# Kernel tuning notes

Hardware: AMD Instinct MI355X
Metric: run time of the kernel (lower is better)

## Reference

```python
import jax, jax.numpy as jnp
import numpy as np

B, N, E = 2, 50000, 400000
C_IN, D, C, S, H, L, FFN = 5, 2, 128, 32, 8, 4, 512
COORD_F, TIME_F, FREQ_BASE, BETA = 8, 4, 1000.0, 1.0
HD = C // H


def setup_inputs() -> dict:
    key = jax.random.key(0)
    ks = jax.random.split(key, 32)
    sc = 0.02
    inp = {
        'inputs': jax.random.normal(ks[0], (B, N, C_IN), jnp.float32),
        'coords': jax.random.uniform(ks[1], (B, N, D), jnp.float32),
        't_norm': jax.random.uniform(ks[2], (B,), jnp.float32),
        'adj_indices': jax.random.randint(ks[3], (2, E), 0, N, jnp.int64 if jax.config.jax_enable_x64 else jnp.int32),
        'adj_values': jax.random.uniform(ks[4], (E,), jnp.float32) * 0.25,  # ~1/avg_degree for stable magnitudes
        'freq_matrix': jax.random.normal(ks[5], (D, COORD_F), jnp.float32),
        'embed_W': jax.random.normal(ks[6], (C_IN + 2 * COORD_F + 2 * TIME_F, C), jnp.float32) * sc,
        'embed_b': jnp.zeros((C,), jnp.float32),
        'ln1_g': jnp.ones((L, C), jnp.float32),
        'ln1_b': jnp.zeros((L, C), jnp.float32),
        'Wslice': jax.random.normal(ks[7], (L, C, S), jnp.float32) * sc,
        'bslice': jnp.zeros((L, S), jnp.float32),
        'Wfront': jax.random.normal(ks[8], (L, C, S), jnp.float32) * sc,
        'bfront': jnp.zeros((L, S), jnp.float32),
        'Win': jax.random.normal(ks[9], (L, C, 3 * C), jnp.float32) * sc,
        'b_in': jnp.zeros((L, 3 * C), jnp.float32),
        'Wout': jax.random.normal(ks[10], (L, C, C), jnp.float32) * sc,
        'bout': jnp.zeros((L, C), jnp.float32),
        'ln2_g': jnp.ones((L, C), jnp.float32),
        'ln2_b': jnp.zeros((L, C), jnp.float32),
        'Wff1': jax.random.normal(ks[11], (L, C, FFN), jnp.float32) * sc,
        'bff1': jnp.zeros((L, FFN), jnp.float32),
        'Wff2': jax.random.normal(ks[12], (L, FFN, C), jnp.float32) * sc,
        'bff2': jnp.zeros((L, C), jnp.float32),
        'proj_W': jax.random.normal(ks[13], (C, C_IN), jnp.float32) * sc,
        'proj_b': jnp.zeros((C_IN,), jnp.float32),
    }
    return inp


def _layer_norm(x, g, b, eps=1e-5):
    m = jnp.mean(x, -1, keepdims=True)
    v = jnp.mean(jnp.square(x - m), -1, keepdims=True)
    return (x - m) * jax.lax.rsqrt(v + eps) * g + b


def _forward(inputs, coords, t_norm, adj_indices, adj_values, freq_matrix,
             embed_W, embed_b, ln1_g, ln1_b, Wslice, bslice, Wfront, bfront,
             Win, b_in, Wout, bout, ln2_g, ln2_b, Wff1, bff1, Wff2, bff2,
             proj_W, proj_b):
    rows, cols = adj_indices[0], adj_indices[1]
    b, n = coords.shape[0], coords.shape[1]
    # spatial Fourier encoding (B,N,2*COORD_F)
    p = 2.0 * jnp.pi * (coords @ freq_matrix)
    sp_enc = jnp.concatenate([jnp.sin(p), jnp.cos(p)], -1)
    # temporal encoding (B,N,2*TIME_F)
    omega = FREQ_BASE ** (-jnp.arange(TIME_F, dtype=jnp.float32) / TIME_F)
    ang = omega[None, :] * (t_norm * FREQ_BASE)[:, None]
    t_enc = jnp.broadcast_to(jnp.concatenate([jnp.sin(ang), jnp.cos(ang)], -1)[:, None, :], (b, n, 2 * TIME_F))
    x = jnp.concatenate([inputs, sp_enc, t_enc], -1) @ embed_W + embed_b  # (B,N,C)
    weights_all = []
    for l in range(L):
        h = _layer_norm(x, ln1_g[l], ln1_b[l])
        # sparse adjacency aggregation: y[r] += a_e * h[c] (duplicates sum == coalesce)
        contrib = adj_values[None, :, None] * h[:, cols, :]  # (B,E,C)
        h_local = jax.vmap(lambda cb: jax.ops.segment_sum(cb, rows, num_segments=n))(contrib)
        h_front = h - h_local
        logits = h @ Wslice[l] + bslice[l] + BETA * (h_front @ Wfront[l] + bfront[l])
        w = jax.nn.softmax(logits, -1)  # (B,N,S)
        wsum = jnp.maximum(jnp.sum(w, axis=1)[:, :, None], 1e-8)  # (B,S,1)
        slices = jnp.einsum('bns,bnc->bsc', w, h) / wsum  # (B,S,C)
        # slice-space MHA (self-attention on S tokens)
        qkv = slices @ Win[l] + b_in[l]
        q, k, v = jnp.split(qkv, 3, axis=-1)
        def split_heads(t):
            return t.reshape(b, S, H, HD).transpose(0, 2, 1, 3)  # (B,H,S,HD)
        qh, kh, vh = split_heads(q), split_heads(k), split_heads(v)
        attn = jax.nn.softmax(jnp.einsum('bhqd,bhkd->bhqk', qh, kh) / jnp.sqrt(jnp.float32(HD)), -1)
        o = jnp.einsum('bhqk,bhkd->bhqd', attn, vh).transpose(0, 2, 1, 3).reshape(b, S, C)
        slices_out = o @ Wout[l] + bout[l]
        x = x + jnp.einsum('bns,bsc->bnc', w, slices_out)
        h2 = _layer_norm(x, ln2_g[l], ln2_b[l])
        x = x + jax.nn.gelu(h2 @ Wff1[l] + bff1[l], approximate=False) @ Wff2[l] + bff2[l]
        weights_all.append(w)
    out = x @ proj_W + proj_b  # (B,N,C_OUT)
    return out, jnp.stack(weights_all)  # (L,B,N,S)


def reference(inputs, coords, t_norm, adj_indices, adj_values, freq_matrix,
              embed_W, embed_b, ln1_g, ln1_b, Wslice, bslice, Wfront, bfront,
              Win, b_in, Wout, bout, ln2_g, ln2_b, Wff1, bff1, Wff2, bff2,
              proj_W, proj_b):
    return _forward(inputs, coords, t_norm, adj_indices, adj_values, freq_matrix,
                    embed_W, embed_b, ln1_g, ln1_b, Wslice, bslice, Wfront, bfront,
                    Win, b_in, Wout, bout, ln2_g, ln2_b, Wff1, bff1, Wff2, bff2,
                    proj_W, proj_b)
```

## Files before the change

### kernel.cpp

```cpp
#include <hip/hip_runtime.h>
#include <math.h>

#define BATCH 2
#define NN 50000
#define NE 400000
#define C_IN 5
#define CC 128
#define SS 32
#define NH 8
#define NL 4
#define FFN 512
#define COORD_F 8
#define TIME_F 4
#define HD 16
#define BETA 1.0f
#define TWO_PI 6.283185307179586476925287f

#define NTOT (BATCH * NN)
#define FF_MT 128
#define FF_BLOCKS ((NTOT + FF_MT - 1) / FF_MT)
#define MPAD (FF_BLOCKS * FF_MT)
#define NBLK ((NN + 127) / 128)
#define LP_PAD 136
#define H2S 136
#define HIDS 72

typedef unsigned short u16;
typedef unsigned int u32;
typedef __attribute__((ext_vector_type(8))) __bf16 bf16x8;
typedef __attribute__((ext_vector_type(4))) float f32x4;

__device__ __forceinline__ u16 f2bf(float f) {
    union { __bf16 b; u16 u; } v;
    v.b = (__bf16)f;
    return v.u;
}

__device__ __forceinline__ float bf2f(u16 h) {
    union { u32 u; float f; } v; v.u = ((u32)h) << 16;
    return v.f;
}

__device__ __forceinline__ float bf_lo(u32 u) {
    union { u32 u; float f; } v; v.u = u << 16;
    return v.f;
}

__device__ __forceinline__ float bf_hi(u32 u) {
    union { u32 u; float f; } v; v.u = u & 0xffff0000u;
    return v.f;
}

__device__ __forceinline__ float gelu_f(float a) {
    float xx = a * 0.7071067811865475f;
    float ax = fabsf(xx);
    float t = 1.0f / fmaf(0.3275911f, ax, 1.0f);
    float poly = t * fmaf(t, fmaf(t, fmaf(t, fmaf(t, 1.061405429f, -1.453152027f),
                                          1.421413741f), -0.284496736f), 0.254829592f);
    float e = __expf(-ax * ax);
    float erfv = copysignf(fmaf(-poly, e, 1.0f), xx);
    return 0.5f * a * (1.0f + erfv);
}

__global__ void count_deg(const int* rows, int* deg) {
    int e = blockIdx.x * blockDim.x + threadIdx.x;
    if (e < NE) atomicAdd(&deg[rows[e]], 1);
}

__global__ __launch_bounds__(512) void scan_deg(const int* deg, int* rowptr) {
    __shared__ int part[512];
    int t = threadIdx.x;
    const int CH = (NN + 511) / 512;
    int begin = t * CH, end = min(begin + CH, NN);
    int s = 0;
    for (int i = begin; i < end; i++) s += deg[i];
    part[t] = s;
    __syncthreads();
    for (int off = 1; off < 512; off <<= 1) {
        int v = (t >= off) ? part[t - off] : 0;
        __syncthreads();
        part[t] += v;
        __syncthreads();
    }
    int base = (t == 0) ? 0 : part[t - 1];
    for (int i = begin; i < end; i++) { rowptr[i] = base; base += deg[i]; }
    if (t == 511) rowptr[NN] = part[511];
}

__global__ void fill_csr(const int* rows, const int* cols, const float* vals,
                         int* cursor, int* csr_col, float* csr_val) {
    int e = blockIdx.x * blockDim.x + threadIdx.x;
    if (e < NE) {
        int p = atomicAdd(&cursor[rows[e]], 1);
        csr_col[p] = cols[e];
        csr_val[p] = vals[e];
    }
}

__global__ __launch_bounds__(128) void embed_ln1_kernel(const float* inputs, const float* coords,
                                                        const float* t_norm, const float* freq,
                                                        const float* W, const float* bias,
                                                        const float* g, const float* bb,
                                                        float* x, u16* hbf) {
    int node = blockIdx.x;
    int b = node / NN;
    int t = threadIdx.x;
    __shared__ float feat[32];
    __shared__ float sm[4];
    if (t < 8) {
        float c0 = coords[node * 2 + 0], c1 = coords[node * 2 + 1];
        float p = TWO_PI * (c0 * freq[t] + c1 * freq[8 + t]);
        feat[5 + t] = sinf(p);
        feat[13 + t] = cosf(p);
    } else if (t < 12) {
        int j = t - 8;
        float omega = powf(1000.0f, -(float)j * 0.25f);
        float ang = omega * t_norm[b] * 1000.0f;
        feat[21 + j] = sinf(ang);
        feat[25 + j] = cosf(ang);
    } else if (t >= 16 && t < 21) {
        feat[t - 16] = inputs[node * 5 + (t - 16)];
    }
    __syncthreads();
    float acc = bias[t];
    #pragma unroll
    for (int k = 0; k < 29; k++) acc += feat[k] * W[k * CC + t];
    x[(size_t)node * CC + t] = acc;
    float s = acc;
    #pragma unroll
    for (int off = 32; off > 0; off >>= 1) s += __shfl_xor(s, off, 64);
    if ((t & 63) == 0) sm[t >> 6] = s;
    __syncthreads();
    float mean = (sm[0] + sm[1]) * (1.0f / 128.0f);
    float d = acc - mean;
    float ss = d * d;
    #pragma unroll
    for (int off = 32; off > 0; off >>= 1) ss += __shfl_xor(ss, off, 64);
    if ((t & 63) == 0) sm[2 + (t >> 6)] = ss;
    __syncthreads();
    float var = (sm[2] + sm[3]) * (1.0f / 128.0f);
    hbf[(size_t)node * CC + t] = f2bf(d * rsqrtf(var + 1e-5f) * g[t] + bb[t]);
}

__global__ __launch_bounds__(256) void agg_kernel(const u16* __restrict__ hbf,
                                                  const int* __restrict__ rowptr,
                                                  const int* __restrict__ csr_col,
                                                  const float* __restrict__ csr_val,
                                                  u16* __restrict__ hlbf) {
    int wid = threadIdx.x >> 6;
    int lane = threadIdx.x & 63;
    int node = blockIdx.x * 4 + wid;
    int b = node / NN, r = node - b * NN;
    int s0 = rowptr[r], s1 = rowptr[r + 1];
    const u32* hb = (const u32*)(hbf + (size_t)b * NN * CC);
    float a0l = 0.f, a1l = 0.f, a2l = 0.f, a3l = 0.f;
    float a0h = 0.f, a1h = 0.f, a2h = 0.f, a3h = 0.f;
    int e = s0;
    for (; e + 4 <= s1; e += 4) {
        int c0 = csr_col[e], c1 = csr_col[e + 1], c2 = csr_col[e + 2], c3 = csr_col[e + 3];
        float v0 = csr_val[e], v1 = csr_val[e + 1], v2 = csr_val[e + 2], v3 = csr_val[e + 3];
        u32 u0 = hb[(size_t)c0 * 64 + lane];
        u32 u1 = hb[(size_t)c1 * 64 + lane];
        u32 u2 = hb[(size_t)c2 * 64 + lane];
        u32 u3 = hb[(size_t)c3 * 64 + lane];
        a0l += v0 * bf_lo(u0);  a0h += v0 * bf_hi(u0);
        a1l += v1 * bf_lo(u1);  a1h += v1 * bf_hi(u1);
        a2l += v2 * bf_lo(u2);  a2h += v2 * bf_hi(u2);
        a3l += v3 * bf_lo(u3);  a3h += v3 * bf_hi(u3);
    }
    for (; e < s1; e++) {
        float v = csr_val[e];
        u32 u = hb[(size_t)csr_col[e] * 64 + lane];
        a0l += v * bf_lo(u);  a0h += v * bf_hi(u);
    }
    float al = (a0l + a1l) + (a2l + a3l);
    float ah = (a0h + a1h) + (a2h + a3h);
    u32 outv = (u32)f2bf(al) | ((u32)f2bf(ah) << 16);
    ((u32*)hlbf)[(size_t)node * 64 + lane] = outv;
}

__global__ __launch_bounds__(256) void pack_logits_weights(const float* Ws, const float* bs,
                                                           const float* Wf, const float* bf,
                                                           u16* Wcombp, float* bcombp) {
    int idx = blockIdx.x * 256 + threadIdx.x;
    if (idx >= NL * SS * 256) return;
    int l = idx / (SS * 256);
    int r = idx - l * (SS * 256);
    int s = r >> 8, k = r & 255;
    float v;
    if (k < 128)
        v = Ws[(size_t)l * CC * SS + (size_t)k * SS + s] + BETA * Wf[(size_t)l * CC * SS + (size_t)k * SS + s];
    else
        v = -BETA * Wf[(size_t)l * CC * SS + (size_t)(k - 128) * SS + s];
    Wcombp[idx] = f2bf(v);
    if (k == 0) bcombp[l * SS + s] = bs[l * SS + s] + BETA * bf[l * SS + s];
}

__global__ __launch_bounds__(256, 2) void logits_pool(const u16* __restrict__ hbf,
                                                      const u16* __restrict__ hlbf,
                                                      const u16* __restrict__ Wcomb,
                                                      const float* __restrict__ bcomb,
                                                      float* __restrict__ wout,
                                                      u16* __restrict__ whi,
                                                      u16* __restrict__ wlo,
                                                      float* __restrict__ slices_acc,
                                                      float* __restrict__ wsum) {
    __shared__ __align__(16) u16 hT[128 * LP_PAD];
    __shared__ __align__(16) u16 wTh[SS * LP_PAD];
    __shared__ __align__(16) u16 wTl[SS * LP_PAD];
    __shared__ float wsum_sh[SS];
    int t = threadIdx.x;
    int b = blockIdx.y;
    int nl0 = blockIdx.x * 128;
    int wv = t >> 6, lane = t & 63;
    int q = lane >> 4, ln16 = lane & 15;
    int nl0w = nl0 + wv * 32;
    if (t < SS) wsum_sh[t] = 0.0f;
    __syncthreads();

    f32x4 acc[2][2];
    #pragma unroll
    for (int mi = 0; mi < 2; mi++)
        #pragma unroll
        for (int ni = 0; ni < 2; ni++) acc[mi][ni] = (f32x4){0.f, 0.f, 0.f, 0.f};

    #pragma unroll
    for (int ks = 0; ks < 8; ks++) {
        const u16* src = (ks < 4) ? hbf : hlbf;
        int ko = (ks & 3) * 32 + q * 8;
        bf16x8 af[2], bfrg[2];
        #pragma unroll
        for (int mi = 0; mi < 2; mi++) {
            int nl = nl0w + mi * 16 + ln16;
            af[mi] = *(const bf16x8*)&src[((size_t)b * NN + nl) * CC + ko];
            if (ks < 4) {
                bool valid = nl < NN;
                const u16* ap = (const u16*)&af[mi];
                int nlb = nl - nl0;
                #pragma unroll
                for (int i = 0; i < 8; i++)
                    hT[(ko + i) * LP_PAD + nlb] = valid ? ap[i] : (u16)0;
            }
        }
        #pragma unroll
        for (int ni = 0; ni < 2; ni++)
            bfrg[ni] = *(const bf16x8*)&Wcomb[(size_t)(ni * 16 + ln16) * 256 + ks * 32 + q * 8];
        #pragma unroll
        for (int mi = 0; mi < 2; mi++)
            #pragma unroll
            for (int ni = 0; ni < 2; ni++)
                acc[mi][ni] = __builtin_amdgcn_mfma_f32_16x16x32_bf16(af[mi], bfrg[ni], acc[mi][ni], 0, 0, 0);
    }

    float bc0 = bcomb[ln16], bc1 = bcomb[16 + ln16];
    float ws0 = 0.0f, ws1 = 0.0f;
    #pragma unroll
    for (int mi = 0; mi < 2; mi++)
        #pragma unroll
        for (int r = 0; r < 4; r++) {
            float l0 = acc[mi][0][r] + bc0;
            float l1 = acc[mi][1][r] + bc1;
            float m = fmaxf(l0, l1);
            #pragma unroll
            for (int msk = 1; msk < 16; msk <<= 1) m = fmaxf(m, __shfl_xor(m, msk, 64));
            float e0 = __expf(l0 - m), e1 = __expf(l1 - m);
            float sum = e0 + e1;
            #pragma unroll
            for (int msk = 1; msk < 16; msk <<= 1) sum += __shfl_xor(sum, msk, 64);
            float is = 1.0f / sum;
            int nl = nl0w + mi * 16 + q * 4 + r;
            bool valid = nl < NN;
            float w0 = valid ? e0 * is : 0.0f;
            float w1 = valid ? e1 * is : 0.0f;
            u16 h0 = f2bf(w0), h1 = f2bf(w1);
            u16 lo0 = f2bf(w0 - bf2f(h0)), lo1 = f2bf(w1 - bf2f(h1));
            if (valid) {
                size_t gb = ((size_t)b * NN + nl) * SS;
                wout[gb + ln16] = w0;
                wout[gb + 16 + ln16] = w1;
                whi[gb + ln16] = h0;  wlo[gb + ln16] = lo0;
                whi[gb + 16 + ln16] = h1;  wlo[gb + 16 + ln16] = lo1;
            }
            int nlb = nl - nl0;
            wTh[ln16 * LP_PAD + nlb] = h0;  wTl[ln16 * LP_PAD + nlb] = lo0;
            wTh[(16 + ln16) * LP_PAD + nlb] = h1;  wTl[(16 + ln16) * LP_PAD + nlb] = lo1;
            ws0 += w0;  ws1 += w1;
        }
    ws0 += __shfl_xor(ws0, 16, 64); ws0 += __shfl_xor(ws0, 32, 64);
    ws1 += __shfl_xor(ws1, 16, 64); ws1 += __shfl_xor(ws1, 32, 64);
    if (q == 0) {
        atomicAdd(&wsum_sh[ln16], ws0);
        atomicAdd(&wsum_sh[16 + ln16], ws1);
    }
    __syncthreads();

    f32x4 pacc[2][8];
    #pragma unroll
    for (int st = 0; st < 2; st++)
        #pragma unroll
        for (int ct = 0; ct < 8; ct++) pacc[st][ct] = (f32x4){0.f, 0.f, 0.f, 0.f};
    {
        int kb = wv * 32 + q * 8;
        bf16x8 wh[2], wl2[2];
        #pragma unroll
        for (int st = 0; st < 2; st++) {
            wh[st] = *(const bf16x8*)&wTh[(st * 16 + ln16) * LP_PAD + kb];
            wl2[st] = *(const bf16x8*)&wTl[(st * 16 + ln16) * LP_PAD + kb];
        }
        #pragma unroll
        for (int ct = 0; ct < 8; ct++) {
            bf16x8 bfr = *(const bf16x8*)&hT[(ct * 16 + ln16) * LP_PAD + kb];
            #pragma unroll
            for (int st = 0; st < 2; st++) {
                pacc[st][ct] = __builtin_amdgcn_mfma_f32_16x16x32_bf16(wh[st], bfr, pacc[st][ct], 0, 0, 0);
                pacc[st][ct] = __builtin_amdgcn_mfma_f32_16x16x32_bf16(wl2[st], bfr, pacc[st][ct], 0, 0, 0);
            }
        }
    }
    __syncthreads();

    float* red = (float*)hT;
    for (int i = t; i < SS * CC; i += 256) red[i] = 0.0f;
    __syncthreads();
    #pragma unroll
    for (int st = 0; st < 2; st++)
        #pragma unroll
        for (int ct = 0; ct < 8; ct++)
            #pragma unroll
            for (int r = 0; r < 4; r++)
                atomicAdd(&red[(st * 16 + q * 4 + r) * CC + ct * 16 + ln16], pacc[st][ct][r]);
    __syncthreads();
    if (t < SS) atomicAdd(&wsum[b * SS + t], wsum_sh[t]);
    #pragma unroll
    for (int k = 0; k < 16; k++) {
        int idx = k * 256 + t;
        atomicAdd(&slices_acc[(size_t)b * SS * CC + idx], red[idx]);
    }
}

__global__ __launch_bounds__(128) void qkv_kernel(const float* slices_acc, const float* wsum,
                                                  const float* Win, const float* b_in_p,
                                                  float* qkv) {
    int blk = blockIdx.x;
    int t = threadIdx.x;
    __shared__ float row[128];
    float iv = 1.0f / fmaxf(wsum[blk], 1e-8f);
    row[t] = slices_acc[(size_t)blk * CC + t] * iv;
    __syncthreads();
    #pragma unroll
    for (int jj = 0; jj < 3; jj++) {
        int j = t + jj * 128;
        float a = b_in_p[j];
        #pragma unroll 8
        for (int c = 0; c < 128; c++) a += row[c] * Win[c * 384 + j];
        qkv[(size_t)blk * 384 + j] = a;
    }
}

__global__ __launch_bounds__(64) void attn_kernel(const float* qkv, float* ovals) {
    int blk = blockIdx.x;
    int b = blk >> 3, h = blk & 7;
    int t = threadIdx.x;
    __shared__ float ksh[32 * 16], vsh[32 * 16];
    for (int i = t; i < 512; i += 64) {
        int k = i >> 4, d = i & 15;
        ksh[i] = qkv[((size_t)b * 32 + k) * 384 + 128 + h * 16 + d];
        vsh[i] = qkv[((size_t)b * 32 + k) * 384 + 256 + h * 16 + d];
    }
    __syncthreads();
    if (t < 32) {
        float qr[16];
        #pragma unroll
        for (int d = 0; d < 16; d++) qr[d] = qkv[((size_t)b * 32 + t) * 384 + h * 16 + d];
        float sc[32];
        float m = -1e30f;
        for (int k = 0; k < 32; k++) {
            float a = 0.0f;
            #pragma unroll
            for (int d = 0; d < 16; d++) a += qr[d] * ksh[k * 16 + d];
            a *= 0.25f;
            sc[k] = a;
            m = fmaxf(m, a);
        }
        float ssum = 0.0f;
        for (int k = 0; k < 32; k++) { float e = expf(sc[k] - m); sc[k] = e; ssum += e; }
        float is = 1.0f / ssum;
        float o[16];
        #pragma unroll
        for (int d = 0; d < 16; d++) o[d] = 0.0f;
        for (int k = 0; k < 32; k++) {
            float p = sc[k] * is;
            #pragma unroll
            for (int d = 0; d < 16; d++) o[d] += p * vsh[k * 16 + d];
        }
        #pragma unroll
        for (int d = 0; d < 16; d++) ovals[((size_t)b * 32 + t) * 128 + h * 16 + d] = o[d];
    }
}

__global__ __launch_bounds__(128) void mha_out_kernel(const float* ovals, const float* Wout,
                                                      const float* bout,
                                                      u16* soThi, u16* soTlo) {
    int blk = blockIdx.x;
    int b = blk >> 5, s = blk & 31;
    int t = threadIdx.x;
    __shared__ float row[128];
    row[t] = ovals[(size_t)blk * 128 + t];
    __syncthreads();
    float a = bout[t];
    #pragma unroll 8
    for (int cc = 0; cc < 128; cc++) a += row[cc] * Wout[cc * CC + t];
    u16 hi = f2bf(a);
    size_t idx = (size_t)b * CC * SS + (size_t)t * SS + s;
    soThi[idx] = hi;
    soTlo[idx] = f2bf(a - bf2f(hi));
}

__global__ __launch_bounds__(256) void pack_ffn_weights(const float* Wff1, const float* Wff2,
                                                        u16* W1p, u16* W2p) {
    int idx = blockIdx.x * 256 + threadIdx.x;
    if (idx >= NL * FFN * CC) return;
    int l = idx / (FFN * CC);
    int r = idx - l * (FFN * CC);
    int j = r >> 7, c = r & 127;
    W1p[idx] = f2bf(Wff1[(size_t)l * CC * FFN + (size_t)c * FFN + j]);
    int c2 = r >> 9, j2 = r & 511;
    W2p[idx] = f2bf(Wff2[(size_t)l * FFN * CC + (size_t)j2 * CC + c2]);
}

__global__ __launch_bounds__(256, 2) void ffn_mega(float* __restrict__ x,
                                                   const u16* __restrict__ whi,
                                                   const u16* __restrict__ wlo,
                                                   const u16* __restrict__ soThi,
                                                   const u16* __restrict__ soTlo,
                                                   const float* __restrict__ g,
                                                   const float* __restrict__ bb,
                                                   const u16* __restrict__ W1p,
                                                   const float* __restrict__ bff1,
                                                   const u16* __restrict__ W2p,
                                                   const float* __restrict__ bff2,
                                                   const float* __restrict__ g1,
                                                   const float* __restrict__ b1,
                                                   u16* __restrict__ hbf_out) {
    __shared__ __align__(16) u16 smem[128 * 144];
    __shared__ __align__(16) float rowst[128 * 4];
    u16* h2t = smem;
    int t = threadIdx.x;
    int b = blockIdx.y;
    int n0 = blockIdx.x * 128;
    int wave = t >> 6, lane = t & 63;
    int wm = wave >> 1, wn = wave & 1;
    int q = lane >> 4, ln16 = lane & 15;
    bool emit = (g1 != nullptr);

    float gr[4], br[4];
    #pragma unroll
    for (int ni = 0; ni < 4; ni++) {
        int col = wn * 64 + ni * 16 + ln16;
        gr[ni] = g[col]; br[ni] = bb[col];
    }

    f32x4 acc2[4][4];
    #pragma unroll
    for (int mi = 0; mi < 4; mi++)
        #pragma unroll
        for (int ni = 0; ni < 4; ni++) acc2[mi][ni] = (f32x4){0.f, 0.f, 0.f, 0.f};

    {
        const u16* soh = soThi + (size_t)b * CC * SS;
        const u16* sol = soTlo + (size_t)b * CC * SS;
        bf16x8 bh[4], bl[4], ah[4], al[4];
        bf16x8 zf;
        #pragma unroll
        for (int i = 0; i < 8; i++) zf[i] = (__bf16)0.0f;
        #pragma unroll
        for (int ni = 0; ni < 4; ni++) {
            int c = wn * 64 + ni * 16 + ln16;
            bh[ni] = *(const bf16x8*)&soh[c * SS + q * 8];
            bl[ni] = *(const bf16x8*)&sol[c * SS + q * 8];
        }
        #pragma unroll
        for (int mi = 0; mi < 4; mi++) {
            int row = n0 + wm * 64 + mi * 16 + ln16;
            if (row < NN) {
                size_t base = ((size_t)b * NN + row) * SS + q * 8;
                ah[mi] = *(const bf16x8*)&whi[base];
                al[mi] = *(const bf16x8*)&wlo[base];
            } else { ah[mi] = zf; al[mi] = zf; }
        }
        #pragma unroll
        for (int mi = 0; mi < 4; mi++)
            #pragma unroll
            for (int ni = 0; ni < 4; ni++) {
                acc2[mi][ni] = __builtin_amdgcn_mfma_f32_16x16x32_bf16(ah[mi], bh[ni], acc2[mi][ni], 0, 0, 0);
                acc2[mi][ni] = __builtin_amdgcn_mfma_f32_16x16x32_bf16(al[mi], bh[ni], acc2[mi][ni], 0, 0, 0);
                acc2[mi][ni] = __builtin_amdgcn_mfma_f32_16x16x32_bf16(ah[mi], bl[ni], acc2[mi][ni], 0, 0, 0);
            }
    }

    #pragma unroll
    for (int mi = 0; mi < 4; mi++)
        #pragma unroll
        for (int r = 0; r < 4; r++) {
            int row = n0 + wm * 64 + mi * 16 + q * 4 + r;
            if (row < NN) {
                const float* xr = &x[((size_t)b * NN + row) * CC + wn * 64 + ln16];
                #pragma unroll
                for (int ni = 0; ni < 4; ni++) acc2[mi][ni][r] += xr[ni * 16];
            }
        }
    #pragma unroll
    for (int mi = 0; mi < 4; mi++)
        #pragma unroll
        for (int r = 0; r < 4; r++) {
            float a = acc2[mi][0][r] + acc2[mi][1][r] + acc2[mi][2][r] + acc2[mi][3][r];
            float a2 = acc2[mi][0][r] * acc2[mi][0][r] + acc2[mi][1][r] * acc2[mi][1][r] +
                       acc2[mi][2][r] * acc2[mi][2][r] + acc2[mi][3][r] * acc2[mi][3][r];
            #pragma unroll
            for (int msk = 1; msk < 16; msk <<= 1) {
                a += __shfl_xor(a, msk, 64);
                a2 += __shfl_xor(a2, msk, 64);
            }
            if (ln16 == 0) {
                int m = wm * 64 + mi * 16 + q * 4 + r;
                rowst[m * 4 + wn * 2] = a;
                rowst[m * 4 + wn * 2 + 1] = a2;
            }
        }
    __syncthreads();
    #pragma unroll
    for (int mi = 0; mi < 4; mi++)
        #pragma unroll
        for (int r = 0; r < 4; r++) {
            int m = wm * 64 + mi * 16 + q * 4 + r;
            float s1 = rowst[m * 4 + 0] + rowst[m * 4 + 2];
            float s2 = rowst[m * 4 + 1] + rowst[m * 4 + 3];
            float mean = s1 * (1.0f / 128.0f);
            float var = s2 * (1.0f / 128.0f) - mean * mean;
            float rstd = rsqrtf(fmaxf(var, 0.0f) + 1e-5f);
            #pragma unroll
            for (int ni = 0; ni < 4; ni++) {
                int col = wn * 64 + ni * 16 + ln16;
                h2t[m * H2S + col] = f2bf((acc2[mi][ni][r] - mean) * rstd * gr[ni] + br[ni]);
            }
        }
    __syncthreads();

    bf16x8 areg[4][4];
    #pragma unroll
    for (int ks = 0; ks < 4; ks++)
        #pragma unroll
        for (int mi = 0; mi < 4; mi++)
            areg[ks][mi] = *(const bf16x8*)&h2t[(wm * 64 + mi * 16 + ln16) * H2S + ks * 32 + q * 8];
    __syncthreads();

    for (int jc = 0; jc < 8; jc++) {
        u16* hid = smem + (jc & 1) * (128 * HIDS);
        f32x4 acc1[4][2];
        #pragma unroll
        for (int mi = 0; mi < 4; mi++)
            #pragma unroll
            for (int ni = 0; ni < 2; ni++) acc1[mi][ni] = (f32x4){0.f, 0.f, 0.f, 0.f};

        __builtin_amdgcn_s_setprio(1);
        #pragma unroll
        for (int ks = 0; ks < 4; ks++) {
            bf16x8 bfr[2];
            #pragma unroll
            for (int ni = 0; ni < 2; ni++)
                bfr[ni] = *(const bf16x8*)&W1p[(size_t)(jc * 64 + wn * 32 + ni * 16 + ln16) * CC + ks * 32 + q * 8];
            #pragma unroll
            for (int mi = 0; mi < 4; mi++)
                #pragma unroll
                for (int ni = 0; ni < 2; ni++)
                    acc1[mi][ni] = __builtin_amdgcn_mfma_f32_16x16x32_bf16(areg[ks][mi], bfr[ni], acc1[mi][ni], 0, 0, 0);
        }
        __builtin_amdgcn_s_setprio(0);

        #pragma unroll
        for (int ni = 0; ni < 2; ni++) {
            float b1v = bff1[jc * 64 + wn * 32 + ni * 16 + ln16];
            #pragma unroll
            for (int mi = 0; mi < 4; mi++)
                #pragma unroll
                for (int r = 0; r < 4; r++)
                    hid[(wm * 64 + mi * 16 + q * 4 + r) * HIDS + wn * 32 + ni * 16 + ln16] =
                        f2bf(gelu_f(acc1[mi][ni][r] + b1v));
        }
        __syncthreads();

        __builtin_amdgcn_s_setprio(1);
        #pragma unroll
        for (int ks2 = 0; ks2 < 2; ks2++) {
            bf16x8 af[4], bfr[4];
            #pragma unroll
            for (int mi = 0; mi < 4; mi++)
                af[mi] = *(const bf16x8*)&hid[(wm * 64 + mi * 16 + ln16) * HIDS + ks2 * 32 + q * 8];
            #pragma unroll
            for (int ni = 0; ni < 4; ni++)
                bfr[ni] = *(const bf16x8*)&W2p[(size_t)(wn * 64 + ni * 16 + ln16) * FFN + jc * 64 + ks2 * 32 + q * 8];
            #pragma unroll
            for (int mi = 0; mi < 4; mi++)
                #pragma unroll
                for (int ni = 0; ni < 4; ni++)
                    acc2[mi][ni] = __builtin_amdgcn_mfma_f32_16x16x32_bf16(af[mi], bfr[ni], acc2[mi][ni], 0, 0, 0);
        }
        __builtin_amdgcn_s_setprio(0);
    }

    float b2[4];
    #pragma unroll
    for (int ni = 0; ni < 4; ni++) b2[ni] = bff2[wn * 64 + ni * 16 + ln16];
    #pragma unroll
    for (int mi = 0; mi < 4; mi++)
        #pragma unroll
        for (int ni = 0; ni < 4; ni++)
            #pragma unroll
            for (int r = 0; r < 4; r++) acc2[mi][ni][r] += b2[ni];

    #pragma unroll
    for (int mi = 0; mi < 4; mi++)
        #pragma unroll
        for (int r = 0; r < 4; r++) {
            int row = n0 + wm * 64 + mi * 16 + q * 4 + r;
            if (row < NN) {
                float* xo = &x[((size_t)b * NN + row) * CC + wn * 64 + ln16];
                #pragma unroll
                for (int ni = 0; ni < 4; ni++) xo[ni * 16] = acc2[mi][ni][r];
            }
        }

    if (emit) {
        float g1r[4], b1r[4];
        #pragma unroll
        for (int ni = 0; ni < 4; ni++) {
            int col = wn * 64 + ni * 16 + ln16;
            g1r[ni] = g1[col]; b1r[ni] = b1[col];
        }
        #pragma unroll
        for (int mi = 0; mi < 4; mi++)
            #pragma unroll
            for (int r = 0; r < 4; r++) {
                float a = acc2[mi][0][r] + acc2[mi][1][r] + acc2[mi][2][r] + acc2[mi][3][r];
                float a2 = acc2[mi][0][r] * acc2[mi][0][r] + acc2[mi][1][r] * acc2[mi][1][r] +
                           acc2[mi][2][r] * acc2[mi][2][r] + acc2[mi][3][r] * acc2[mi][3][r];
                #pragma unroll
                for (int msk = 1; msk < 16; msk <<= 1) {
                    a += __shfl_xor(a, msk, 64);
                    a2 += __shfl_xor(a2, msk, 64);
                }
                if (ln16 == 0) {
                    int m = wm * 64 + mi * 16 + q * 4 + r;
                    rowst[m * 4 + wn * 2] = a;
                    rowst[m * 4 + wn * 2 + 1] = a2;
                }
            }
        __syncthreads();
        #pragma unroll
        for (int mi = 0; mi < 4; mi++)
            #pragma unroll
            for (int r = 0; r < 4; r++) {
                int m = wm * 64 + mi * 16 + q * 4 + r;
                float s1 = rowst[m * 4 + 0] + rowst[m * 4 + 2];
                float s2 = rowst[m * 4 + 1] + rowst[m * 4 + 3];
                float mean = s1 * (1.0f / 128.0f);
                float var = s2 * (1.0f / 128.0f) - mean * mean;
                float rstd = rsqrtf(fmaxf(var, 0.0f) + 1e-5f);
                #pragma unroll
                for (int ni = 0; ni < 4; ni++) {
                    int col = wn * 64 + ni * 16 + ln16;
                    smem[m * H2S + col] = f2bf((acc2[mi][ni][r] - mean) * rstd * g1r[ni] + b1r[ni]);
                }
            }
        __syncthreads();
        #pragma unroll
        for (int it = 0; it < 8; it++) {
            int chunk = it * 256 + t;
            int m = chunk >> 4;
            int c8 = (chunk & 15) << 3;
            int row = n0 + m;
            if (row < NN)
                *(f32x4*)&hbf_out[((size_t)b * NN + row) * CC + c8] =
                    *(const f32x4*)&smem[m * H2S + c8];
        }
    }
}

__global__ __launch_bounds__(128) void proj_kernel(const float* x, const float* W,
                                                   const float* bias, float* outp) {
    int node = blockIdx.x;
    int t = threadIdx.x;
    __shared__ float xr[128];
    __shared__ float pr[40];
    xr[t] = x[(size_t)node * CC + t];
    __syncthreads();
    if (t < 40) {
        int k = t / 8, part = t % 8;
        float a = 0.0f;
        #pragma unroll
        for (int i = 0; i < 16; i++) {
            int c = part * 16 + i;
            a += xr[c] * W[c * C_IN + k];
        }
        pr[t] = a;
    }
    __syncthreads();
    if (t < 5) {
        float a = bias[t];
        #pragma unroll
        for (int p = 0; p < 8; p++) a += pr[t * 8 + p];
        outp[(size_t)node * C_IN + t] = a;
    }
}

extern "C" void kernel_launch(void* const* d_in, const int* in_sizes, int n_in,
                              void* d_out, int out_size, void* d_ws, size_t ws_size,
                              hipStream_t stream) {
    const float* inputs  = (const float*)d_in[0];
    const float* coords  = (const float*)d_in[1];
    const float* t_norm  = (const float*)d_in[2];
    const int*   adj     = (const int*)d_in[3];
    const float* adj_v   = (const float*)d_in[4];
    const float* freq    = (const float*)d_in[5];
    const float* embed_W = (const float*)d_in[6];
    const float* embed_b = (const float*)d_in[7];
    const float* ln1_g   = (const float*)d_in[8];
    const float* ln1_b   = (const float*)d_in[9];
    const float* Wslice  = (const float*)d_in[10];
    const float* bslice  = (const float*)d_in[11];
    const float* Wfront  = (const float*)d_in[12];
    const float* bfront  = (const float*)d_in[13];
    const float* Win     = (const float*)d_in[14];
    const float* b_in    = (const float*)d_in[15];
    const float* Wout    = (const float*)d_in[16];
    const float* bout    = (const float*)d_in[17];
    const float* ln2_g   = (const float*)d_in[18];
    const float* ln2_b   = (const float*)d_in[19];
    const float* Wff1    = (const float*)d_in[20];
    const float* bff1    = (const float*)d_in[21];
    const float* Wff2    = (const float*)d_in[22];
    const float* bff2    = (const float*)d_in[23];
    const float* proj_W  = (const float*)d_in[24];
    const float* proj_b  = (const float*)d_in[25];

    float* out = (float*)d_out;
    float* wout_base = out + (size_t)BATCH * NN * C_IN;

    float* x          = (float*)d_ws;
    u16*   hbf        = (u16*)(x + (size_t)NTOT * CC);
    u16*   hlbf       = hbf + (size_t)MPAD * CC;
    u16*   whi        = hlbf + (size_t)MPAD * CC;
    u16*   wlo        = whi + (size_t)(NTOT + 128) * SS;
    u16*   soThi      = wlo + (size_t)(NTOT + 128) * SS;
    u16*   soTlo      = soThi + BATCH * CC * SS;
    float* slices_acc = (float*)(soTlo + BATCH * CC * SS);
    float* wsum       = slices_acc + BATCH * SS * CC;
    float* qkv_ws     = wsum + BATCH * SS;
    float* ovals_ws   = qkv_ws + BATCH * SS * 384;
    float* csr_val    = ovals_ws + BATCH * SS * CC;
    int*   rowptr     = (int*)(csr_val + NE);
    int*   cursor     = rowptr + (NN + 1);
    int*   deg        = cursor + NN;
    int*   csr_col    = deg + NN;
    u16*   W1p        = (u16*)(csr_col + NE);
    u16*   W2p        = W1p + NL * FFN * CC;
    u16*   Wcombp     = W2p + NL * CC * FFN;
    float* bcomb      = (float*)(Wcombp + NL * SS * 256);

    hipMemsetAsync(deg, 0, NN * sizeof(int), stream);
    count_deg<<<(NE + 255) / 256, 256, 0, stream>>>(adj, deg);
    scan_deg<<<1, 512, 0, stream>>>(deg, rowptr);
    hipMemcpyAsync(cursor, rowptr, NN * sizeof(int), hipMemcpyDeviceToDevice, stream);
    fill_csr<<<(NE + 255) / 256, 256, 0, stream>>>(adj, adj + NE, adj_v, cursor, csr_col, csr_val);

    pack_ffn_weights<<<(NL * FFN * CC + 255) / 256, 256, 0, stream>>>(Wff1, Wff2, W1p, W2p);
    pack_logits_weights<<<(NL * SS * 256 + 255) / 256, 256, 0, stream>>>(Wslice, bslice, Wfront,
                                                                         bfront, Wcombp, bcomb);

    embed_ln1_kernel<<<NTOT, 128, 0, stream>>>(inputs, coords, t_norm, freq, embed_W, embed_b,
                                               ln1_g, ln1_b, x, hbf);

    for (int l = 0; l < NL; l++) {
        float* wl = wout_base + (size_t)l * NTOT * SS;
        agg_kernel<<<NTOT / 4, 256, 0, stream>>>(hbf, rowptr, csr_col, csr_val, hlbf);
        hipMemsetAsync(slices_acc, 0, (BATCH * SS * CC + BATCH * SS) * sizeof(float), stream);
        dim3 glp(NBLK, BATCH);
        logits_pool<<<glp, 256, 0, stream>>>(hbf, hlbf, Wcombp + (size_t)l * SS * 256,
                                             bcomb + l * SS, wl, whi, wlo, slices_acc, wsum);
        qkv_kernel<<<BATCH * SS, 128, 0, stream>>>(slices_acc, wsum,
                                                   Win + (size_t)l * CC * 3 * CC,
                                                   b_in + l * 3 * CC, qkv_ws);
        attn_kernel<<<BATCH * NH, 64, 0, stream>>>(qkv_ws, ovals_ws);
        mha_out_kernel<<<BATCH * SS, 128, 0, stream>>>(ovals_ws, Wout + (size_t)l * CC * CC,
                                                       bout + l * CC, soThi, soTlo);
        const float* g1n = (l + 1 < NL) ? (ln1_g + (size_t)(l + 1) * CC) : nullptr;
        const float* b1n = (l + 1 < NL) ? (ln1_b + (size_t)(l + 1) * CC) : nullptr;
        dim3 g3(NBLK, BATCH);
        ffn_mega<<<g3, 256, 0, stream>>>(x, whi, wlo, soThi, soTlo,
                                         ln2_g + l * CC, ln2_b + l * CC,
                                         W1p + (size_t)l * FFN * CC, bff1 + l * FFN,
                                         W2p + (size_t)l * CC * FFN, bff2 + l * CC,
                                         g1n, b1n, hbf);
    }

    proj_kernel<<<NTOT, 128, 0, stream>>>(x, proj_W, proj_b, out);
}
```

Measured before the change: 1.767 ms.

## Batch nodes per block in embed/proj and spread slice atomics over replicas

The embedding+LN1 kernel now handles 8 nodes per block, with the 29 weights cached in registers, and the projection kernel handles 12 nodes per block. Both changes cut the per-node block launch overhead that came from one block per node. The logits_pool atomics into slices_acc are spread across 16 replica buffers, which a new reduce_slices kernel then sums. This reduces atomic contention at the cost of an extra memset, an extra kernel launch and more register pressure.

```diff
diff --git a/kernel.cpp b/kernel.cpp
--- a/kernel.cpp
+++ b/kernel.cpp
@@ -24,6 +24,9 @@
 #define LP_PAD 136
 #define H2S 136
 #define HIDS 72
+#define NREP 16
+#define EMB_NPB 8
+#define PROJ_NPB 12
 
 typedef unsigned short u16;
 typedef unsigned int u32;
@@ -97,49 +100,85 @@
     }
 }
 
-__global__ __launch_bounds__(128) void embed_ln1_kernel(const float* inputs, const float* coords,
-                                                        const float* t_norm, const float* freq,
-                                                        const float* W, const float* bias,
-                                                        const float* g, const float* bb,
-                                                        float* x, u16* hbf) {
-    int node = blockIdx.x;
-    int b = node / NN;
+__global__ __launch_bounds__(128) void embed_ln1_kernel(const float* __restrict__ inputs,
+                                                        const float* __restrict__ coords,
+                                                        const float* __restrict__ t_norm,
+                                                        const float* __restrict__ freq,
+                                                        const float* __restrict__ W,
+                                                        const float* __restrict__ bias,
+                                                        const float* __restrict__ g,
+                                                        const float* __restrict__ bb,
+                                                        float* __restrict__ x,
+                                                        u16* __restrict__ hbf) {
     int t = threadIdx.x;
-    __shared__ float feat[32];
-    __shared__ float sm[4];
-    if (t < 8) {
-        float c0 = coords[node * 2 + 0], c1 = coords[node * 2 + 1];
-        float p = TWO_PI * (c0 * freq[t] + c1 * freq[8 + t]);
-        feat[5 + t] = sinf(p);
-        feat[13 + t] = cosf(p);
-    } else if (t < 12) {
-        int j = t - 8;
-        float omega = powf(1000.0f, -(float)j * 0.25f);
-        float ang = omega * t_norm[b] * 1000.0f;
-        feat[21 + j] = sinf(ang);
-        feat[25 + j] = cosf(ang);
-    } else if (t >= 16 && t < 21) {
-        feat[t - 16] = inputs[node * 5 + (t - 16)];
-    }
-    __syncthreads();
-    float acc = bias[t];
-    #pragma unroll
-    for (int k = 0; k < 29; k++) acc += feat[k] * W[k * CC + t];
-    x[(size_t)node * CC + t] = acc;
-    float s = acc;
-    #pragma unroll
-    for (int off = 32; off > 0; off >>= 1) s += __shfl_xor(s, off, 64);
-    if ((t & 63) == 0) sm[t >> 6] = s;
-    __syncthreads();
-    float mean = (sm[0] + sm[1]) * (1.0f / 128.0f);
-    float d = acc - mean;
-    float ss = d * d;
-    #pragma unroll
-    for (int off = 32; off > 0; off >>= 1) ss += __shfl_xor(ss, off, 64);
-    if ((t & 63) == 0) sm[2 + (t >> 6)] = ss;
-    __syncthreads();
-    float var = (sm[2] + sm[3]) * (1.0f / 128.0f);
-    hbf[(size_t)node * CC + t] = f2bf(d * rsqrtf(var + 1e-5f) * g[t] + bb[t]);
+    int n0 = blockIdx.x * EMB_NPB;
+    __shared__ float feat[EMB_NPB][32];
+    __shared__ float sm[EMB_NPB][4];
+    if (t < EMB_NPB) {
+        int node = n0 + t;
+        if (node < NTOT) {
+            int b = node / NN;
+            float c0 = coords[node * 2 + 0], c1 = coords[node * 2 + 1];
+            #pragma unroll
+            for (int j = 0; j < 8; j++) {
+                float p = TWO_PI * (c0 * freq[j] + c1 * freq[8 + j]);
+                feat[t][5 + j] = sinf(p);
+                feat[t][13 + j] = cosf(p);
+            }
+            #pragma unroll
+            for (int j = 0; j < 4; j++) {
+                float omega = powf(1000.0f, -(float)j * 0.25f);
+                float ang = omega * t_norm[b] * 1000.0f;
+                feat[t][21 + j] = sinf(ang);
+                feat[t][25 + j] = cosf(ang);
+            }
+            #pragma unroll
+            for (int k = 0; k < 5; k++) feat[t][k] = inputs[node * 5 + k];
+        }
+    }
+    float Wr[29];
+    #pragma unroll
+    for (int k = 0; k < 29; k++) Wr[k] = W[k * CC + t];
+    float bi = bias[t], gt = g[t], bbt = bb[t];
+    __syncthreads();
+    float accv[EMB_NPB];
+    #pragma unroll
+    for (int nn = 0; nn < EMB_NPB; nn++) {
+        float a = bi;
+        #pragma unroll
+        for (int k = 0; k < 29; k++) a += feat[nn][k] * Wr[k];
+        accv[nn] = a;
+        int node = n0 + nn;
+        if (node < NTOT) x[(size_t)node * CC + t] = a;
+    }
+    #pragma unroll
+    for (int nn = 0; nn < EMB_NPB; nn++) {
+        float s = accv[nn];
+        #pragma unroll
+        for (int off = 32; off > 0; off >>= 1) s += __shfl_xor(s, off, 64);
+        if ((t & 63) == 0) sm[nn][t >> 6] = s;
+    }
+    __syncthreads();
+    float dv[EMB_NPB];
+    #pragma unroll
+    for (int nn = 0; nn < EMB_NPB; nn++) {
+        float mean = (sm[nn][0] + sm[nn][1]) * (1.0f / 128.0f);
+        float d = accv[nn] - mean;
+        dv[nn] = d;
+        float ss = d * d;
+        #pragma unroll
+        for (int off = 32; off > 0; off >>= 1) ss += __shfl_xor(ss, off, 64);
+        if ((t & 63) == 0) sm[nn][2 + (t >> 6)] = ss;
+    }
+    __syncthreads();
+    #pragma unroll
+    for (int nn = 0; nn < EMB_NPB; nn++) {
+        int node = n0 + nn;
+        if (node < NTOT) {
+            float var = (sm[nn][2] + sm[nn][3]) * (1.0f / 128.0f);
+            hbf[(size_t)node * CC + t] = f2bf(dv[nn] * rsqrtf(var + 1e-5f) * gt + bbt);
+        }
+    }
 }
 
 __global__ __launch_bounds__(256) void agg_kernel(const u16* __restrict__ hbf,
@@ -203,7 +242,7 @@
                                                       float* __restrict__ wout,
                                                       u16* __restrict__ whi,
                                                       u16* __restrict__ wlo,
-                                                      float* __restrict__ slices_acc,
+                                                      float* __restrict__ rep,
                                                       float* __restrict__ wsum) {
     __shared__ __align__(16) u16 hT[128 * LP_PAD];
     __shared__ __align__(16) u16 wTh[SS * LP_PAD];
@@ -331,11 +370,24 @@
                 atomicAdd(&red[(st * 16 + q * 4 + r) * CC + ct * 16 + ln16], pacc[st][ct][r]);
     __syncthreads();
     if (t < SS) atomicAdd(&wsum[b * SS + t], wsum_sh[t]);
+    int rep_id = (blockIdx.y * NBLK + blockIdx.x) & (NREP - 1);
+    float* dst = rep + ((size_t)rep_id * BATCH + b) * SS * CC;
     #pragma unroll
     for (int k = 0; k < 16; k++) {
         int idx = k * 256 + t;
-        atomicAdd(&slices_acc[(size_t)b * SS * CC + idx], red[idx]);
-    }
+        atomicAdd(&dst[idx], red[idx]);
+    }
+}
+
+__global__ __launch_bounds__(256) void reduce_slices(const float* __restrict__ rep,
+                                                     float* __restrict__ slices_acc) {
+    int j = blockIdx.x * 256 + threadIdx.x;
+    int b = j >> 12;
+    int e = j & 4095;
+    float s = 0.0f;
+    #pragma unroll
+    for (int r = 0; r < NREP; r++) s += rep[((size_t)r * BATCH + b) * SS * CC + e];
+    slices_acc[(size_t)b * SS * CC + e] = s;
 }
 
 __global__ __launch_bounds__(128) void qkv_kernel(const float* slices_acc, const float* wsum,
@@ -686,30 +738,44 @@
     }
 }
 
-__global__ __launch_bounds__(128) void proj_kernel(const float* x, const float* W,
-                                                   const float* bias, float* outp) {
-    int node = blockIdx.x;
+__global__ __launch_bounds__(128) void proj_kernel(const float* __restrict__ x,
+                                                   const float* __restrict__ W,
+                                                   const float* __restrict__ bias,
+                                                   float* __restrict__ outp) {
     int t = threadIdx.x;
-    __shared__ float xr[128];
-    __shared__ float pr[40];
-    xr[t] = x[(size_t)node * CC + t];
-    __syncthreads();
-    if (t < 40) {
-        int k = t / 8, part = t % 8;
-        float a = 0.0f;
-        #pragma unroll
-        for (int i = 0; i < 16; i++) {
-            int c = part * 16 + i;
-            a += xr[c] * W[c * C_IN + k];
-        }
-        pr[t] = a;
-    }
-    __syncthreads();
-    if (t < 5) {
-        float a = bias[t];
-        #pragma unroll
-        for (int p = 0; p < 8; p++) a += pr[t * 8 + p];
-        outp[(size_t)node * C_IN + t] = a;
+    int n0 = blockIdx.x * PROJ_NPB;
+    __shared__ float xr[PROJ_NPB][128];
+    __shared__ float pr[3][40];
+    for (int idx = t; idx < PROJ_NPB * 128; idx += 128) {
+        int nn = idx >> 7, c = idx & 127;
+        int node = n0 + nn;
+        xr[nn][c] = (node < NTOT) ? x[(size_t)node * CC + c] : 0.0f;
+    }
+    __syncthreads();
+    for (int pass = 0; pass < 4; pass++) {
+        if (t < 120) {
+            int nl = t / 40, tt = t - nl * 40;
+            int k = tt / 8, part = tt % 8;
+            float a = 0.0f;
+            #pragma unroll
+            for (int i = 0; i < 16; i++) {
+                int c = part * 16 + i;
+                a += xr[pass * 3 + nl][c] * W[c * C_IN + k];
+            }
+            pr[nl][tt] = a;
+        }
+        __syncthreads();
+        if (t < 15) {
+            int nl = t / 5, k = t - nl * 5;
+            int node = n0 + pass * 3 + nl;
+            if (node < NTOT) {
+                float a = bias[k];
+                #pragma unroll
+                for (int p = 0; p < 8; p++) a += pr[nl][k * 8 + p];
+                outp[(size_t)node * C_IN + k] = a;
+            }
+        }
+        __syncthreads();
     }
 }
 
@@ -766,6 +832,7 @@
     u16*   W2p        = W1p + NL * FFN * CC;
     u16*   Wcombp     = W2p + NL * CC * FFN;
     float* bcomb      = (float*)(Wcombp + NL * SS * 256);
+    float* rep        = bcomb + NL * SS;
 
     hipMemsetAsync(deg, 0, NN * sizeof(int), stream);
     count_deg<<<(NE + 255) / 256, 256, 0, stream>>>(adj, deg);
@@ -777,16 +844,18 @@
     pack_logits_weights<<<(NL * SS * 256 + 255) / 256, 256, 0, stream>>>(Wslice, bslice, Wfront,
                                                                          bfront, Wcombp, bcomb);
 
-    embed_ln1_kernel<<<NTOT, 128, 0, stream>>>(inputs, coords, t_norm, freq, embed_W, embed_b,
-                                               ln1_g, ln1_b, x, hbf);
+    embed_ln1_kernel<<<(NTOT + EMB_NPB - 1) / EMB_NPB, 128, 0, stream>>>(
+        inputs, coords, t_norm, freq, embed_W, embed_b, ln1_g, ln1_b, x, hbf);
 
     for (int l = 0; l < NL; l++) {
         float* wl = wout_base + (size_t)l * NTOT * SS;
         agg_kernel<<<NTOT / 4, 256, 0, stream>>>(hbf, rowptr, csr_col, csr_val, hlbf);
-        hipMemsetAsync(slices_acc, 0, (BATCH * SS * CC + BATCH * SS) * sizeof(float), stream);
+        hipMemsetAsync(rep, 0, (size_t)NREP * BATCH * SS * CC * sizeof(float), stream);
+        hipMemsetAsync(wsum, 0, BATCH * SS * sizeof(float), stream);
         dim3 glp(NBLK, BATCH);
         logits_pool<<<glp, 256, 0, stream>>>(hbf, hlbf, Wcombp + (size_t)l * SS * 256,
-                                             bcomb + l * SS, wl, whi, wlo, slices_acc, wsum);
+                                             bcomb + l * SS, wl, whi, wlo, rep, wsum);
+        reduce_slices<<<(BATCH * SS * CC) / 256, 256, 0, stream>>>(rep, slices_acc);
         qkv_kernel<<<BATCH * SS, 128, 0, stream>>>(slices_acc, wsum,
                                                    Win + (size_t)l * CC * 3 * CC,
                                                    b_in + l * 3 * CC, qkv_ws);
@@ -803,5 +872,5 @@
                                          g1n, b1n, hbf);
     }
 
-    proj_kernel<<<NTOT, 128, 0, stream>>>(x, proj_W, proj_b, out);
-}
+    proj_kernel<<<(NTOT + PROJ_NPB - 1) / PROJ_NPB, 128, 0, stream>>>(x, proj_W, proj_b, out);
+}
```

Result: no change. 1.764 ms (-0.2%).
